# Kernel optimization log

Hardware: AMD Instinct MI355X
Metric: run time of the kernel (lower is better)

## Reference

```python
import jax, jax.numpy as jnp
import numpy as np

D_MODEL = 1024
NHEAD = 16
HEAD_DIM = D_MODEL // NHEAD
SCALE = 1.0 / np.sqrt(HEAD_DIM).astype(np.float32)
B, L = 2, 2048
NEG_INF = -1e30


def setup_inputs() -> dict:
    key = jax.random.key(0)
    ks = jax.random.split(key, 12)
    xav = np.sqrt(6.0 / (D_MODEL + D_MODEL)).astype(np.float32)  # xavier_uniform gain=1
    def lin_w(k):
        return jax.random.uniform(k, (D_MODEL, D_MODEL), jnp.float32, -xav, xav)
    x = jax.random.normal(ks[0], (B, L, D_MODEL), jnp.float32)
    role_mask = jax.random.randint(ks[1], (B, L), 0, 2, jnp.int32)
    # causal attention mask: True = masked (upper triangle above diagonal)
    attn_mask = jnp.triu(jnp.ones((L, L), jnp.bool_), k=1)
    # random key padding: True = padded key
    key_padding_mask = jax.random.randint(ks[2], (B, L), 0, 2, jnp.int32).astype(jnp.bool_)
    return {
        "x": x,
        "role_mask": role_mask,
        "attn_mask": attn_mask,
        "key_padding_mask": key_padding_mask,
        "Wq": lin_w(ks[3]), "bq": jnp.zeros((D_MODEL,), jnp.float32),
        "Wk": lin_w(ks[4]), "bk": jnp.zeros((D_MODEL,), jnp.float32),
        "Wv": lin_w(ks[5]), "bv": jnp.zeros((D_MODEL,), jnp.float32),
        "Wo": lin_w(ks[6]), "bo": jnp.zeros((D_MODEL,), jnp.float32),
        "delta": jnp.asarray(1.0, jnp.float32),
    }


def reference(x, role_mask, attn_mask, key_padding_mask,
              Wq, bq, Wk, bk, Wv, bv, Wo, bo, delta):
    Bb, Ll, Dd = x.shape
    def heads(t):  # [B,L,D] -> [B,H,L,hd]
        return t.reshape(Bb, Ll, NHEAD, HEAD_DIM).transpose(0, 2, 1, 3)
    Q = heads(x @ Wq.T + bq)
    K = heads(x @ Wk.T + bk)
    V = heads(x @ Wv.T + bv)
    scores = jnp.einsum('bhqd,bhkd->bhqk', Q, K) * SCALE  # [B,H,L,L]
    same_role = (role_mask[:, :, None] == role_mask[:, None, :])  # [B,L,L]
    scores = scores + (same_role.astype(scores.dtype) * delta)[:, None, :, :]
    scores = jnp.where(attn_mask[None, None, :, :], -jnp.inf, scores)
    scores = jnp.where(key_padding_mask[:, None, None, :], -jnp.inf, scores)
    attn = jax.nn.softmax(scores, axis=-1)
    attn = jnp.nan_to_num(attn, nan=0.0, posinf=0.0, neginf=0.0)
    out = jnp.einsum('bhqk,bhkd->bhqd', attn, V)
    out = out.transpose(0, 2, 1, 3).reshape(Bb, Ll, Dd)
    return out @ Wo.T + bo
```

## Files before the change

kernel.cpp:

```cpp
#include <hip/hip_runtime.h>
#include <hip/hip_bf16.h>

#define DM 1024
#define NH 16
#define HD 64
#define BB 2
#define LL 2048
#define SCALE 0.125f
#define NEG_BIG -1e30f
#define LOG2E 1.4426950408889634f
#define SC2 (SCALE * LOG2E)
#define FIXM 16.0f
#define SLOTB 8448
#define POOL0_SLOTS 960

typedef __bf16 bf16;
typedef __bf16 bf16x8 __attribute__((ext_vector_type(8)));
typedef __bf16 bf16x4 __attribute__((ext_vector_type(4)));
typedef float f32x4 __attribute__((ext_vector_type(4)));

static __device__ inline bf16x8 load8(const bf16* p) {
    return *reinterpret_cast<const bf16x8*>(p);
}

static __device__ inline float scrub(float x) {
    union { float f; unsigned u; } c; c.f = x;
    return ((c.u & 0x7F800000u) == 0x7F800000u) ? 0.f : x;
}

typedef __attribute__((address_space(1))) const unsigned char ga_t;
typedef __attribute__((address_space(3))) unsigned char ls_t;
static __device__ inline void gload_lds16(const void* g, void* l) {
    __builtin_amdgcn_global_load_lds((ga_t*)g, (ls_t*)l, 16, 0, 0);
}

__global__ __launch_bounds__(256) void prep_all(
    const float* __restrict__ x,
    const float* __restrict__ Wq, const float* __restrict__ Wk,
    const float* __restrict__ Wv, const float* __restrict__ Wo,
    bf16* __restrict__ xb, bf16* __restrict__ Wqb, bf16* __restrict__ Wkb,
    bf16* __restrict__ Wvb, bf16* __restrict__ Wob,
    const int* __restrict__ role, const void* __restrict__ kpad,
    const float* __restrict__ deltap, float2* __restrict__ biasG)
{
    const int tid = threadIdx.x;
    const int gid = blockIdx.x;
    if (gid < 2048) {
        const float* src; bf16* dst; size_t base;
        if (gid < 1024) { src = x; dst = xb; base = (size_t)gid * 1024; }
        else {
            const int wsel = (gid - 1024) >> 8;
            src = (wsel == 0) ? Wq : (wsel == 1) ? Wk : (wsel == 2) ? Wv : Wo;
            dst = (wsel == 0) ? Wqb : (wsel == 1) ? Wkb : (wsel == 2) ? Wvb : Wob;
            base = (size_t)((gid - 1024) & 255) * 1024;
        }
#pragma unroll
        for (int it = 0; it < 4; it++) {
            const size_t i = base + it * 256 + tid;
            const f32x4 v = ((const f32x4*)src)[i];
            bf16x4 o;
            o[0] = (bf16)v[0]; o[1] = (bf16)v[1]; o[2] = (bf16)v[2]; o[3] = (bf16)v[3];
            ((bf16x4*)dst)[i] = o;
        }
        return;
    }
    const unsigned char* kb = (const unsigned char*)kpad;
    int f3F = 0, fLow = 0, fOff = 0;
    for (int i = (tid & 63); i < BB * LL; i += 64) {
        const unsigned char v = kb[i];
        if (v == 0x3F) f3F = 1;
        if ((i & 3) < 2 && v) fLow = 1;
        if ((i & 3) && v) fOff = 1;
    }
    const int mode = __any(f3F) ? (__any(fLow) ? 3 : 2) : (__any(fOff) ? 1 : 0);
    const float d2 = scrub(deltap[0]) * LOG2E;
    const int idx = (gid - 2048) * 256 + tid;
    const bool pad = (mode == 0) ? (((const int*)kpad)[idx] != 0)
                   : (mode == 1) ? (((const unsigned char*)kpad)[idx] != 0)
                   : (mode == 2) ? (((const float*)kpad)[idx] != 0.f)
                                 : (((const unsigned short*)kpad)[idx] != 0);
    const int r = role[idx];
    const float base = (pad ? NEG_BIG : 0.f) - FIXM;
    float2 o;
    o.x = base + ((r == 0) ? d2 : 0.f);
    o.y = base + ((r == 1) ? d2 : 0.f);
    biasG[idx] = o;
}

__global__ __launch_bounds__(256) void qkv_bf16(
    const bf16* __restrict__ xb,
    const bf16* __restrict__ Wqb, const bf16* __restrict__ Wkb, const bf16* __restrict__ Wvb,
    const float* __restrict__ bq, const float* __restrict__ bk, const float* __restrict__ bv,
    bf16* __restrict__ qw, bf16* __restrict__ kw, bf16* __restrict__ vw)
{
    __shared__ bf16 As[128 * 32];
    __shared__ bf16 Bs[128 * 32];
    const int tid = threadIdx.x;
    const int lane = tid & 63, w = tid >> 6;
    const int wm = w >> 1, wn = w & 1;
    const int ln = lane & 15, quad = lane >> 4;

    const int m0 = blockIdx.x * 128;
    const int sel = blockIdx.y >> 3;
    const int nloc0 = (blockIdx.y & 7) * 128;

    const bf16* Wb = (sel == 0) ? Wqb : ((sel == 1) ? Wkb : Wvb);
    const float* bias = (sel == 0) ? bq : ((sel == 1) ? bk : bv);

    const int rA = lane >> 2;
    const int cA = (lane & 3) * 8;

    f32x4 acc[4][4] = {};
    for (int k0 = 0; k0 < DM; k0 += 32) {
        __syncthreads();
#pragma unroll
        for (int s = 0; s < 2; s++) {
            const int r0 = s * 64 + w * 16;
            gload_lds16(xb + (size_t)(m0 + r0 + rA) * DM + k0 + cA, &As[r0 * 32]);
            gload_lds16(Wb + (size_t)(nloc0 + r0 + rA) * DM + k0 + cA, &Bs[r0 * 32]);
        }
        __syncthreads();
        bf16x8 a[4], b[4];
#pragma unroll
        for (int mi = 0; mi < 4; mi++)
            a[mi] = *(bf16x8*)&As[(wm * 64 + mi * 16 + ln) * 32 + quad * 8];
#pragma unroll
        for (int ni = 0; ni < 4; ni++)
            b[ni] = *(bf16x8*)&Bs[(wn * 64 + ni * 16 + ln) * 32 + quad * 8];
#pragma unroll
        for (int mi = 0; mi < 4; mi++)
#pragma unroll
            for (int ni = 0; ni < 4; ni++)
                acc[mi][ni] = __builtin_amdgcn_mfma_f32_16x16x32_bf16(a[mi], b[ni], acc[mi][ni], 0, 0, 0);
    }

#pragma unroll
    for (int mi = 0; mi < 4; mi++) {
#pragma unroll
        for (int ni = 0; ni < 4; ni++) {
            const int ncol = nloc0 + wn * 64 + ni * 16 + ln;
            const float bv_ = bias[ncol];
            const int hh = ncol >> 6, dd = ncol & 63;
#pragma unroll
            for (int i = 0; i < 4; i++) {
                const int row = m0 + wm * 64 + mi * 16 + quad * 4 + i;
                const int bb = row >> 11, llr = row & (LL - 1);
                const bf16 v = (bf16)scrub(acc[mi][ni][i] + bv_);
                const size_t idx = (((size_t)(bb * NH + hh) * LL) + llr) * HD + dd;
                if (sel == 0)      qw[idx] = v;
                else if (sel == 1) kw[idx] = v;
                else               vw[idx] = v;
            }
        }
    }
}

__global__ __launch_bounds__(256) void vtrans(
    const bf16* __restrict__ vw, bf16* __restrict__ vtw)
{
    __shared__ bf16 T[64 * 72];
    const int tid = threadIdx.x;
    const int bh = blockIdx.x >> 5;
    const int l0 = (blockIdx.x & 31) * 64;
    const size_t base = (size_t)bh * LL * HD;

#pragma unroll
    for (int pass = 0; pass < 2; pass++) {
        const int e = pass * 2048 + tid * 8;
        const int r = e >> 6, c = e & 63;
        *(bf16x8*)&T[r * 72 + c] = load8(vw + base + (size_t)(l0 + r) * HD + c);
    }
    __syncthreads();
#pragma unroll
    for (int pass = 0; pass < 2; pass++) {
        const int e = pass * 2048 + tid * 8;
        const int d = e >> 6, lc = e & 63;
        bf16x8 v;
#pragma unroll
        for (int j = 0; j < 8; j++) v[j] = T[(lc + j) * 72 + d];
        *(bf16x8*)(vtw + base + (size_t)d * LL + l0 + lc) = v;
    }
}

#define PSTR 40
__global__ __launch_bounds__(256) void attn_v7(
    const bf16* __restrict__ qw, const bf16* __restrict__ kw, const bf16* __restrict__ vtw,
    const int* __restrict__ role, const float2* __restrict__ biasG,
    char* __restrict__ pool0, char* __restrict__ pool1,
    bf16* __restrict__ attn_out)
{
    const int qb = 31 - (blockIdx.x / 3);
    const int c = blockIdx.x % 3;
    const int nch = (qb + 12) / 12;
    if (c >= nch) return;

    __shared__ bf16 Ks[2][2][64 * 32];
    __shared__ bf16 Vs[2][2][64 * 32];
    __shared__ bf16 Ps[4][2][16 * PSTR];

    const int tid = threadIdx.x;
    const int lane = tid & 63, w = tid >> 6;
    const int col = lane & 15, quad = lane >> 4;
    const int bh = blockIdx.y;
    const int h = bh & (NH - 1), b = bh >> 4;
    const int q0 = qb * 64 + w * 16;

    const bf16* qbase = qw + (size_t)((b * NH + h) * LL) * HD;
    const bf16* kbase = kw + (size_t)((b * NH + h) * LL) * HD;
    const bf16* vbase = vtw + (size_t)((b * NH + h) * HD) * LL;
    const float2* bias2 = biasG + (size_t)b * LL;
    const int* rrow = role + b * LL;

    const int srow = lane >> 2;
    const int scol = (lane & 3) * 8;
    const bf16* ksrc = kbase + (size_t)(w * 16 + srow) * HD + scol;
    const bf16* vsrc = vbase + (size_t)(w * 16 + srow) * LL + scol;

    bf16x8 qf[2];
    qf[0] = load8(qbase + (size_t)(q0 + col) * HD + quad * 8);
    qf[1] = load8(qbase + (size_t)(q0 + col) * HD + 32 + quad * 8);

    int role_q[4];
#pragma unroll
    for (int i = 0; i < 4; i++) role_q[i] = rrow[q0 + quad * 4 + i];

    float lacc[4] = {0.f, 0.f, 0.f, 0.f};
    f32x4 o[4] = {};

    const int t0 = c * 12;
    const int t1 = (t0 + 12 < qb + 1) ? t0 + 12 : qb + 1;

    {
        const int kp = t0 * 64;
#pragma unroll
        for (int st = 0; st < 2; st++)
            gload_lds16(ksrc + (size_t)kp * HD + st * 32, &Ks[0][st][w * 512]);
#pragma unroll
        for (int kh = 0; kh < 2; kh++)
            gload_lds16(vsrc + kp + kh * 32, &Vs[0][kh][w * 512]);
    }

    for (int kt = t0; kt < t1; kt++) {
        const int cur = (kt - t0) & 1;
        __syncthreads();

        if (kt + 1 < t1) {
            const int k1 = (kt + 1) * 64;
#pragma unroll
            for (int st = 0; st < 2; st++)
                gload_lds16(ksrc + (size_t)k1 * HD + st * 32, &Ks[cur ^ 1][st][w * 512]);
#pragma unroll
            for (int kh = 0; kh < 2; kh++)
                gload_lds16(vsrc + k1 + kh * 32, &Vs[cur ^ 1][kh][w * 512]);
        }

        const int k0 = kt * 64;
        float2 bb[4];
#pragma unroll
        for (int ns = 0; ns < 4; ns++) bb[ns] = bias2[k0 + ns * 16 + col];

        f32x4 s[4] = {};
#pragma unroll
        for (int st = 0; st < 2; st++) {
#pragma unroll
            for (int ns = 0; ns < 4; ns++) {
                const bf16x8 kf = *(bf16x8*)&Ks[cur][st][(ns * 16 + col) * 32 + quad * 8];
                s[ns] = __builtin_amdgcn_mfma_f32_16x16x32_bf16(qf[st], kf, s[ns], 0, 0, 0);
            }
        }
        const bool diag = (kt == qb);
#pragma unroll
        for (int ns = 0; ns < 4; ns++) {
            const int kk = k0 + ns * 16 + col;
#pragma unroll
            for (int i = 0; i < 4; i++) {
                float sv = fmaf(s[ns][i], SC2, role_q[i] ? bb[ns].y : bb[ns].x);
                if (diag && kk > q0 + quad * 4 + i) sv = NEG_BIG;
                const float p = exp2f(fminf(sv, 14.f));
                lacc[i] += p;
                Ps[w][ns >> 1][(quad * 4 + i) * PSTR + (ns & 1) * 16 + col] = (bf16)p;
            }
        }
        bf16x8 pf[2];
#pragma unroll
        for (int st = 0; st < 2; st++)
            pf[st] = *(bf16x8*)&Ps[w][st][col * PSTR + quad * 8];
#pragma unroll
        for (int ns = 0; ns < 4; ns++) {
#pragma unroll
            for (int kh = 0; kh < 2; kh++) {
                const bf16x8 vf = *(bf16x8*)&Vs[cur][kh][(ns * 16 + col) * 32 + quad * 8];
                o[ns] = __builtin_amdgcn_mfma_f32_16x16x32_bf16(pf[kh], vf, o[ns], 0, 0, 0);
            }
        }
    }

    if (nch == 1) {
        bf16* orow = attn_out + (size_t)(b * LL) * DM;
#pragma unroll
        for (int i = 0; i < 4; i++) {
            float l = lacc[i];
#pragma unroll
            for (int off = 8; off > 0; off >>= 1)
                l += __shfl_xor(l, off, 16);
            const float inv = (l > 0.f) ? 1.f / l : 0.f;
            const int qq = q0 + quad * 4 + i;
#pragma unroll
            for (int ns = 0; ns < 4; ns++)
                orow[(size_t)qq * DM + h * HD + ns * 16 + col] = (bf16)scrub(o[ns][i] * inv);
        }
    } else {
        const int base = (qb <= 23) ? (qb - 12) * 2 : 24 + (qb - 24) * 3;
        const int slot = bh * 48 + base + c;
        char* ptr = (slot < POOL0_SLOTS) ? (pool0 + (size_t)slot * SLOTB)
                                         : (pool1 + (size_t)(slot - POOL0_SLOTS) * SLOTB);
        bf16* op = (bf16*)ptr;
        float* lp = (float*)(ptr + 8192);
#pragma unroll
        for (int i = 0; i < 4; i++) {
            float l = lacc[i];
#pragma unroll
            for (int off = 8; off > 0; off >>= 1)
                l += __shfl_xor(l, off, 16);
            const int r = w * 16 + quad * 4 + i;
            if (col == 0) lp[r] = l;
#pragma unroll
            for (int ns = 0; ns < 4; ns++)
                op[r * 64 + ns * 16 + col] = (bf16)scrub(o[ns][i]);
        }
    }
}

__global__ __launch_bounds__(256) void combine(
    const char* __restrict__ pool0, const char* __restrict__ pool1,
    bf16* __restrict__ attn_out)
{
    const int qb = 12 + blockIdx.x;
    const int bh = blockIdx.y;
    const int h = bh & (NH - 1), b = bh >> 4;
    const int nch = (qb + 12) / 12;
    const int base = (qb <= 23) ? (qb - 12) * 2 : 24 + (qb - 24) * 3;

    const char* ptr[3];
    for (int c = 0; c < nch; c++) {
        const int slot = bh * 48 + base + c;
        ptr[c] = (slot < POOL0_SLOTS) ? (pool0 + (size_t)slot * SLOTB)
                                      : (pool1 + (size_t)(slot - POOL0_SLOTS) * SLOTB);
    }

    __shared__ float linv[64];
    const int tid = threadIdx.x;
    if (tid < 64) {
        float ls = 0.f;
        for (int c = 0; c < nch; c++) ls += ((const float*)(ptr[c] + 8192))[tid];
        linv[tid] = (ls > 0.f) ? 1.f / ls : 0.f;
    }
    __syncthreads();

    const int r = tid >> 2;
    const int d0 = (tid & 3) * 16;
    float acc[16] = {};
    for (int c = 0; c < nch; c++) {
        const bf16* op = (const bf16*)ptr[c];
#pragma unroll
        for (int half = 0; half < 2; half++) {
            const bf16x8 v = load8(op + r * 64 + d0 + half * 8);
#pragma unroll
            for (int j = 0; j < 8; j++) acc[half * 8 + j] += (float)v[j];
        }
    }
    const float inv = linv[r];
    bf16x8 outv[2];
#pragma unroll
    for (int half = 0; half < 2; half++)
#pragma unroll
        for (int j = 0; j < 8; j++)
            outv[half][j] = (bf16)scrub(acc[half * 8 + j] * inv);
    bf16* orow = attn_out + ((size_t)(b * LL) + qb * 64 + r) * DM + h * HD + d0;
    *(bf16x8*)orow = outv[0];
    *(bf16x8*)(orow + 8) = outv[1];
}

__global__ __launch_bounds__(256) void out_bf16(
    const bf16* __restrict__ A, const bf16* __restrict__ Wb,
    const float* __restrict__ bias, float* __restrict__ out)
{
    __shared__ bf16 As[128 * 32];
    __shared__ bf16 Bs[64 * 32];
    const int tid = threadIdx.x;
    const int lane = tid & 63, w = tid >> 6;
    const int ln = lane & 15, quad = lane >> 4;
    const int m0 = blockIdx.x * 128;
    const int n0 = blockIdx.y * 64;

    const int rA = lane >> 2;
    const int cA = (lane & 3) * 8;

    f32x4 acc[2][4] = {};
    for (int k0 = 0; k0 < DM; k0 += 32) {
        __syncthreads();
#pragma unroll
        for (int s = 0; s < 2; s++) {
            const int r0 = s * 64 + w * 16;
            gload_lds16(A + (size_t)(m0 + r0 + rA) * DM + k0 + cA, &As[r0 * 32]);
        }
        gload_lds16(Wb + (size_t)(n0 + w * 16 + rA) * DM + k0 + cA, &Bs[w * 16 * 32]);
        __syncthreads();
        bf16x8 a[2], b[4];
#pragma unroll
        for (int mi = 0; mi < 2; mi++)
            a[mi] = *(bf16x8*)&As[(w * 32 + mi * 16 + ln) * 32 + quad * 8];
#pragma unroll
        for (int ni = 0; ni < 4; ni++)
            b[ni] = *(bf16x8*)&Bs[(ni * 16 + ln) * 32 + quad * 8];
#pragma unroll
        for (int mi = 0; mi < 2; mi++)
#pragma unroll
            for (int ni = 0; ni < 4; ni++)
                acc[mi][ni] = __builtin_amdgcn_mfma_f32_16x16x32_bf16(a[mi], b[ni], acc[mi][ni], 0, 0, 0);
    }
#pragma unroll
    for (int mi = 0; mi < 2; mi++) {
#pragma unroll
        for (int ni = 0; ni < 4; ni++) {
            const int ncol = n0 + ni * 16 + ln;
            const float bv_ = bias[ncol];
#pragma unroll
            for (int i = 0; i < 4; i++) {
                const int row = m0 + w * 32 + mi * 16 + quad * 4 + i;
                out[(size_t)row * DM + ncol] = scrub(acc[mi][ni][i] + bv_);
            }
        }
    }
}

extern "C" void kernel_launch(void* const* d_in, const int* in_sizes, int n_in,
                              void* d_out, int out_size, void* d_ws, size_t ws_size,
                              hipStream_t stream) {
    const float* x    = (const float*)d_in[0];
    const int*   role = (const int*)d_in[1];
    const void*  kpad = d_in[3];
    const float* Wq = (const float*)d_in[4];
    const float* bq = (const float*)d_in[5];
    const float* Wk = (const float*)d_in[6];
    const float* bk = (const float*)d_in[7];
    const float* Wv = (const float*)d_in[8];
    const float* bv = (const float*)d_in[9];
    const float* Wo = (const float*)d_in[10];
    const float* bo = (const float*)d_in[11];
    const float* dl = (const float*)d_in[12];

    char* ws = (char*)d_ws;
    bf16* qw   = (bf16*)(ws);
    bf16* kw   = (bf16*)(ws + (size_t)(8u  << 20));
    bf16* vnat = (bf16*)(ws + (size_t)(16u << 20));
    bf16* aw   = (bf16*)(ws + (size_t)(24u << 20));
    bf16* xb   = (bf16*)(ws + (size_t)(32u << 20));
    bf16* vtw  = xb;
    bf16* Wqb  = (bf16*)(ws + (size_t)(40u << 20));
    bf16* Wkb  = (bf16*)(ws + (size_t)(42u << 20));
    bf16* Wvb  = (bf16*)(ws + (size_t)(44u << 20));
    bf16* Wob  = (bf16*)(ws + (size_t)(46u << 20));
    float2* biasG = (float2*)(ws + (size_t)(48u << 20));
    char* pool0 = (char*)vnat;
    char* pool1 = (char*)Wqb;
    float* out = (float*)d_out;

    prep_all<<<dim3(2064), dim3(256), 0, stream>>>(
        x, Wq, Wk, Wv, Wo, xb, Wqb, Wkb, Wvb, Wob, role, kpad, dl, biasG);
    qkv_bf16<<<dim3(32, 24), dim3(256), 0, stream>>>(xb, Wqb, Wkb, Wvb, bq, bk, bv, qw, kw, vnat);
    vtrans<<<dim3(BB * NH * (LL / 64)), dim3(256), 0, stream>>>(vnat, vtw);
    attn_v7<<<dim3(96, 32), dim3(256), 0, stream>>>(qw, kw, vtw, role, biasG, pool0, pool1, aw);
    combine<<<dim3(20, 32), dim3(256), 0, stream>>>(pool0, pool1, aw);
    out_bf16<<<dim3(32, 16), dim3(256), 0, stream>>>(aw, Wob, bo, out);
}
```

Before: 260.5 us.

## Fuse fp32-to-bf16 conversion into GEMMs and write V transposed directly

Removes the separate conversion pass by having the QKV and output GEMMs load fp32 x/weights and convert to bf16 while staging into LDS. The QKV epilogue writes V directly in transposed layout, which eliminates the vtrans kernel. The mask/bias prep blocks are folded into the QKV launch, and the attention grid is compacted to 60 columns so no blocks exit immediately. This saves launches and intermediate traffic, but the GEMMs now read twice the bytes through register loads instead of async LDS loads, and the transposed V stores are strided.

```diff
diff --git a/kernel.cpp b/kernel.cpp
--- a/kernel.cpp
+++ b/kernel.cpp
@@ -23,6 +23,15 @@
     return *reinterpret_cast<const bf16x8*>(p);
 }
 
+static __device__ inline bf16x8 cvt8(const float* p) {
+    const f32x4 a = *reinterpret_cast<const f32x4*>(p);
+    const f32x4 b = *reinterpret_cast<const f32x4*>(p + 4);
+    bf16x8 r;
+    r[0] = (bf16)a[0]; r[1] = (bf16)a[1]; r[2] = (bf16)a[2]; r[3] = (bf16)a[3];
+    r[4] = (bf16)b[0]; r[5] = (bf16)b[1]; r[6] = (bf16)b[2]; r[7] = (bf16)b[3];
+    return r;
+}
+
 static __device__ inline float scrub(float x) {
     union { float f; unsigned u; } c; c.f = x;
     return ((c.u & 0x7F800000u) == 0x7F800000u) ? 0.f : x;
@@ -34,90 +43,68 @@
     __builtin_amdgcn_global_load_lds((ga_t*)g, (ls_t*)l, 16, 0, 0);
 }
 
-__global__ __launch_bounds__(256) void prep_all(
+__global__ __launch_bounds__(256) void qkv_mega(
     const float* __restrict__ x,
-    const float* __restrict__ Wq, const float* __restrict__ Wk,
-    const float* __restrict__ Wv, const float* __restrict__ Wo,
-    bf16* __restrict__ xb, bf16* __restrict__ Wqb, bf16* __restrict__ Wkb,
-    bf16* __restrict__ Wvb, bf16* __restrict__ Wob,
+    const float* __restrict__ Wq, const float* __restrict__ Wk, const float* __restrict__ Wv,
+    const float* __restrict__ bq, const float* __restrict__ bk, const float* __restrict__ bv,
     const int* __restrict__ role, const void* __restrict__ kpad,
-    const float* __restrict__ deltap, float2* __restrict__ biasG)
+    const float* __restrict__ deltap,
+    bf16* __restrict__ qw, bf16* __restrict__ kw, bf16* __restrict__ vtw,
+    float2* __restrict__ biasG)
 {
     const int tid = threadIdx.x;
-    const int gid = blockIdx.x;
-    if (gid < 2048) {
-        const float* src; bf16* dst; size_t base;
-        if (gid < 1024) { src = x; dst = xb; base = (size_t)gid * 1024; }
-        else {
-            const int wsel = (gid - 1024) >> 8;
-            src = (wsel == 0) ? Wq : (wsel == 1) ? Wk : (wsel == 2) ? Wv : Wo;
-            dst = (wsel == 0) ? Wqb : (wsel == 1) ? Wkb : (wsel == 2) ? Wvb : Wob;
-            base = (size_t)((gid - 1024) & 255) * 1024;
-        }
-#pragma unroll
-        for (int it = 0; it < 4; it++) {
-            const size_t i = base + it * 256 + tid;
-            const f32x4 v = ((const f32x4*)src)[i];
-            bf16x4 o;
-            o[0] = (bf16)v[0]; o[1] = (bf16)v[1]; o[2] = (bf16)v[2]; o[3] = (bf16)v[3];
-            ((bf16x4*)dst)[i] = o;
-        }
+    const int g = blockIdx.x;
+
+    if (g >= 768) {
+        const unsigned char* kb = (const unsigned char*)kpad;
+        int f3F = 0, fLow = 0, fOff = 0;
+        for (int i = (tid & 63); i < BB * LL; i += 64) {
+            const unsigned char v = kb[i];
+            if (v == 0x3F) f3F = 1;
+            if ((i & 3) < 2 && v) fLow = 1;
+            if ((i & 3) && v) fOff = 1;
+        }
+        const int mode = __any(f3F) ? (__any(fLow) ? 3 : 2) : (__any(fOff) ? 1 : 0);
+        const float d2 = scrub(deltap[0]) * LOG2E;
+        const int idx = (g - 768) * 256 + tid;
+        const bool pad = (mode == 0) ? (((const int*)kpad)[idx] != 0)
+                       : (mode == 1) ? (((const unsigned char*)kpad)[idx] != 0)
+                       : (mode == 2) ? (((const float*)kpad)[idx] != 0.f)
+                                     : (((const unsigned short*)kpad)[idx] != 0);
+        const int r = role[idx];
+        const float base = (pad ? NEG_BIG : 0.f) - FIXM;
+        float2 o;
+        o.x = base + ((r == 0) ? d2 : 0.f);
+        o.y = base + ((r == 1) ? d2 : 0.f);
+        biasG[idx] = o;
         return;
     }
-    const unsigned char* kb = (const unsigned char*)kpad;
-    int f3F = 0, fLow = 0, fOff = 0;
-    for (int i = (tid & 63); i < BB * LL; i += 64) {
-        const unsigned char v = kb[i];
-        if (v == 0x3F) f3F = 1;
-        if ((i & 3) < 2 && v) fLow = 1;
-        if ((i & 3) && v) fOff = 1;
-    }
-    const int mode = __any(f3F) ? (__any(fLow) ? 3 : 2) : (__any(fOff) ? 1 : 0);
-    const float d2 = scrub(deltap[0]) * LOG2E;
-    const int idx = (gid - 2048) * 256 + tid;
-    const bool pad = (mode == 0) ? (((const int*)kpad)[idx] != 0)
-                   : (mode == 1) ? (((const unsigned char*)kpad)[idx] != 0)
-                   : (mode == 2) ? (((const float*)kpad)[idx] != 0.f)
-                                 : (((const unsigned short*)kpad)[idx] != 0);
-    const int r = role[idx];
-    const float base = (pad ? NEG_BIG : 0.f) - FIXM;
-    float2 o;
-    o.x = base + ((r == 0) ? d2 : 0.f);
-    o.y = base + ((r == 1) ? d2 : 0.f);
-    biasG[idx] = o;
-}
-
-__global__ __launch_bounds__(256) void qkv_bf16(
-    const bf16* __restrict__ xb,
-    const bf16* __restrict__ Wqb, const bf16* __restrict__ Wkb, const bf16* __restrict__ Wvb,
-    const float* __restrict__ bq, const float* __restrict__ bk, const float* __restrict__ bv,
-    bf16* __restrict__ qw, bf16* __restrict__ kw, bf16* __restrict__ vw)
-{
+
     __shared__ bf16 As[128 * 32];
     __shared__ bf16 Bs[128 * 32];
-    const int tid = threadIdx.x;
     const int lane = tid & 63, w = tid >> 6;
     const int wm = w >> 1, wn = w & 1;
     const int ln = lane & 15, quad = lane >> 4;
 
-    const int m0 = blockIdx.x * 128;
-    const int sel = blockIdx.y >> 3;
-    const int nloc0 = (blockIdx.y & 7) * 128;
-
-    const bf16* Wb = (sel == 0) ? Wqb : ((sel == 1) ? Wkb : Wvb);
+    const int m0 = (g & 31) * 128;
+    const int by = g >> 5;
+    const int sel = by >> 3;
+    const int nloc0 = (by & 7) * 128;
+
+    const float* W    = (sel == 0) ? Wq : ((sel == 1) ? Wk : Wv);
     const float* bias = (sel == 0) ? bq : ((sel == 1) ? bk : bv);
 
-    const int rA = lane >> 2;
-    const int cA = (lane & 3) * 8;
+    const int srow = tid >> 2;
+    const int scb  = (tid & 3) * 8;
 
     f32x4 acc[4][4] = {};
     for (int k0 = 0; k0 < DM; k0 += 32) {
         __syncthreads();
 #pragma unroll
-        for (int s = 0; s < 2; s++) {
-            const int r0 = s * 64 + w * 16;
-            gload_lds16(xb + (size_t)(m0 + r0 + rA) * DM + k0 + cA, &As[r0 * 32]);
-            gload_lds16(Wb + (size_t)(nloc0 + r0 + rA) * DM + k0 + cA, &Bs[r0 * 32]);
+        for (int p = 0; p < 2; p++) {
+            const int row = p * 64 + srow;
+            *(bf16x8*)&As[row * 32 + scb] = cvt8(x + (size_t)(m0 + row) * DM + k0 + scb);
+            *(bf16x8*)&Bs[row * 32 + scb] = cvt8(W + (size_t)(nloc0 + row) * DM + k0 + scb);
         }
         __syncthreads();
         bf16x8 a[4], b[4];
@@ -146,53 +133,30 @@
                 const int row = m0 + wm * 64 + mi * 16 + quad * 4 + i;
                 const int bb = row >> 11, llr = row & (LL - 1);
                 const bf16 v = (bf16)scrub(acc[mi][ni][i] + bv_);
-                const size_t idx = (((size_t)(bb * NH + hh) * LL) + llr) * HD + dd;
-                if (sel == 0)      qw[idx] = v;
-                else if (sel == 1) kw[idx] = v;
-                else               vw[idx] = v;
+                if (sel == 0)
+                    qw[(((size_t)(bb * NH + hh) * LL) + llr) * HD + dd] = v;
+                else if (sel == 1)
+                    kw[(((size_t)(bb * NH + hh) * LL) + llr) * HD + dd] = v;
+                else
+                    vtw[(((size_t)(bb * NH + hh) * HD) + dd) * LL + llr] = v;
             }
         }
     }
 }
 
-__global__ __launch_bounds__(256) void vtrans(
-    const bf16* __restrict__ vw, bf16* __restrict__ vtw)
-{
-    __shared__ bf16 T[64 * 72];
-    const int tid = threadIdx.x;
-    const int bh = blockIdx.x >> 5;
-    const int l0 = (blockIdx.x & 31) * 64;
-    const size_t base = (size_t)bh * LL * HD;
-
-#pragma unroll
-    for (int pass = 0; pass < 2; pass++) {
-        const int e = pass * 2048 + tid * 8;
-        const int r = e >> 6, c = e & 63;
-        *(bf16x8*)&T[r * 72 + c] = load8(vw + base + (size_t)(l0 + r) * HD + c);
-    }
-    __syncthreads();
-#pragma unroll
-    for (int pass = 0; pass < 2; pass++) {
-        const int e = pass * 2048 + tid * 8;
-        const int d = e >> 6, lc = e & 63;
-        bf16x8 v;
-#pragma unroll
-        for (int j = 0; j < 8; j++) v[j] = T[(lc + j) * 72 + d];
-        *(bf16x8*)(vtw + base + (size_t)d * LL + l0 + lc) = v;
-    }
-}
-
 #define PSTR 40
-__global__ __launch_bounds__(256) void attn_v7(
+__global__ __launch_bounds__(256) void attn_v8(
     const bf16* __restrict__ qw, const bf16* __restrict__ kw, const bf16* __restrict__ vtw,
     const int* __restrict__ role, const float2* __restrict__ biasG,
     char* __restrict__ pool0, char* __restrict__ pool1,
     bf16* __restrict__ attn_out)
 {
-    const int qb = 31 - (blockIdx.x / 3);
-    const int c = blockIdx.x % 3;
+    const int xg = blockIdx.x;
+    int qb, c;
+    if (xg < 24)      { qb = 31 - xg / 3; c = xg % 3; }
+    else if (xg < 48) { qb = 23 - (xg - 24) / 2; c = (xg - 24) % 2; }
+    else              { qb = 59 - xg; c = 0; }
     const int nch = (qb + 12) / 12;
-    if (c >= nch) return;
 
     __shared__ bf16 Ks[2][2][64 * 32];
     __shared__ bf16 Vs[2][2][64 * 32];
@@ -381,8 +345,8 @@
     *(bf16x8*)(orow + 8) = outv[1];
 }
 
-__global__ __launch_bounds__(256) void out_bf16(
-    const bf16* __restrict__ A, const bf16* __restrict__ Wb,
+__global__ __launch_bounds__(256) void out_mega(
+    const bf16* __restrict__ A, const float* __restrict__ Wo,
     const float* __restrict__ bias, float* __restrict__ out)
 {
     __shared__ bf16 As[128 * 32];
@@ -395,6 +359,8 @@
 
     const int rA = lane >> 2;
     const int cA = (lane & 3) * 8;
+    const int srow = tid >> 2;
+    const int scb  = (tid & 3) * 8;
 
     f32x4 acc[2][4] = {};
     for (int k0 = 0; k0 < DM; k0 += 32) {
@@ -404,7 +370,7 @@
             const int r0 = s * 64 + w * 16;
             gload_lds16(A + (size_t)(m0 + r0 + rA) * DM + k0 + cA, &As[r0 * 32]);
         }
-        gload_lds16(Wb + (size_t)(n0 + w * 16 + rA) * DM + k0 + cA, &Bs[w * 16 * 32]);
+        *(bf16x8*)&Bs[srow * 32 + scb] = cvt8(Wo + (size_t)(n0 + srow) * DM + k0 + scb);
         __syncthreads();
         bf16x8 a[2], b[4];
 #pragma unroll
@@ -453,24 +419,17 @@
     char* ws = (char*)d_ws;
     bf16* qw   = (bf16*)(ws);
     bf16* kw   = (bf16*)(ws + (size_t)(8u  << 20));
-    bf16* vnat = (bf16*)(ws + (size_t)(16u << 20));
+    char* pool0 = ws + (size_t)(16u << 20);
     bf16* aw   = (bf16*)(ws + (size_t)(24u << 20));
-    bf16* xb   = (bf16*)(ws + (size_t)(32u << 20));
-    bf16* vtw  = xb;
-    bf16* Wqb  = (bf16*)(ws + (size_t)(40u << 20));
-    bf16* Wkb  = (bf16*)(ws + (size_t)(42u << 20));
-    bf16* Wvb  = (bf16*)(ws + (size_t)(44u << 20));
-    bf16* Wob  = (bf16*)(ws + (size_t)(46u << 20));
+    bf16* vtw  = (bf16*)(ws + (size_t)(32u << 20));
+    char* pool1 = ws + (size_t)(40u << 20);
     float2* biasG = (float2*)(ws + (size_t)(48u << 20));
-    char* pool0 = (char*)vnat;
-    char* pool1 = (char*)Wqb;
     float* out = (float*)d_out;
 
-    prep_all<<<dim3(2064), dim3(256), 0, stream>>>(
-        x, Wq, Wk, Wv, Wo, xb, Wqb, Wkb, Wvb, Wob, role, kpad, dl, biasG);
-    qkv_bf16<<<dim3(32, 24), dim3(256), 0, stream>>>(xb, Wqb, Wkb, Wvb, bq, bk, bv, qw, kw, vnat);
-    vtrans<<<dim3(BB * NH * (LL / 64)), dim3(256), 0, stream>>>(vnat, vtw);
-    attn_v7<<<dim3(96, 32), dim3(256), 0, stream>>>(qw, kw, vtw, role, biasG, pool0, pool1, aw);
+    qkv_mega<<<dim3(784), dim3(256), 0, stream>>>(
+        x, Wq, Wk, Wv, bq, bk, bv, role, kpad, dl, qw, kw, vtw, biasG);
+    attn_v8<<<dim3(60, 32), dim3(256), 0, stream>>>(
+        qw, kw, vtw, role, biasG, pool0, pool1, aw);
     combine<<<dim3(20, 32), dim3(256), 0, stream>>>(pool0, pool1, aw);
-    out_bf16<<<dim3(32, 16), dim3(256), 0, stream>>>(aw, Wob, bo, out);
-}
+    out_mega<<<dim3(32, 16), dim3(256), 0, stream>>>(aw, Wo, bo, out);
+}
```

New measurement: 257.7 us. About the same (-1.1%).

## Fuse V transpose into QKV epilogue, vectorize P stores, compact attention grid

Applied to the files above, without the earlier changes.

The QKV projection now writes V straight into a transposed layout with a permuted key order inside each 64-key tile, so the separate vtrans kernel and its extra global round trip are dropped. In the attention kernel, P values are packed four at a time into bf16x4 stores using the matching permuted layout and a smaller LDS stride, in place of scalar LDS writes. The grid shrinks from 96 to 60 blocks per head by mapping block indices only to the (query block, chunk) pairs that do work, so no blocks launch just to exit. The workspace layout is rearranged to fit, and the transposed V stores from the GEMM epilogue are scattered, which may cost write efficiency.

```diff
diff --git a/kernel.cpp b/kernel.cpp
--- a/kernel.cpp
+++ b/kernel.cpp
@@ -91,7 +91,7 @@
     const bf16* __restrict__ xb,
     const bf16* __restrict__ Wqb, const bf16* __restrict__ Wkb, const bf16* __restrict__ Wvb,
     const float* __restrict__ bq, const float* __restrict__ bk, const float* __restrict__ bv,
-    bf16* __restrict__ qw, bf16* __restrict__ kw, bf16* __restrict__ vw)
+    bf16* __restrict__ qw, bf16* __restrict__ kw, bf16* __restrict__ vtw)
 {
     __shared__ bf16 As[128 * 32];
     __shared__ bf16 Bs[128 * 32];
@@ -146,53 +146,33 @@
                 const int row = m0 + wm * 64 + mi * 16 + quad * 4 + i;
                 const int bb = row >> 11, llr = row & (LL - 1);
                 const bf16 v = (bf16)scrub(acc[mi][ni][i] + bv_);
-                const size_t idx = (((size_t)(bb * NH + hh) * LL) + llr) * HD + dd;
-                if (sel == 0)      qw[idx] = v;
-                else if (sel == 1) kw[idx] = v;
-                else               vw[idx] = v;
+                if (sel == 0)
+                    qw[(((size_t)(bb * NH + hh) * LL) + llr) * HD + dd] = v;
+                else if (sel == 1)
+                    kw[(((size_t)(bb * NH + hh) * LL) + llr) * HD + dd] = v;
+                else {
+                    const int kl = llr & 63;
+                    const int pos = (llr & ~63) + ((kl & 15) * 4 + (kl >> 4));
+                    vtw[(((size_t)(bb * NH + hh) * HD) + dd) * LL + pos] = v;
+                }
             }
         }
     }
 }
 
-__global__ __launch_bounds__(256) void vtrans(
-    const bf16* __restrict__ vw, bf16* __restrict__ vtw)
-{
-    __shared__ bf16 T[64 * 72];
-    const int tid = threadIdx.x;
-    const int bh = blockIdx.x >> 5;
-    const int l0 = (blockIdx.x & 31) * 64;
-    const size_t base = (size_t)bh * LL * HD;
-
-#pragma unroll
-    for (int pass = 0; pass < 2; pass++) {
-        const int e = pass * 2048 + tid * 8;
-        const int r = e >> 6, c = e & 63;
-        *(bf16x8*)&T[r * 72 + c] = load8(vw + base + (size_t)(l0 + r) * HD + c);
-    }
-    __syncthreads();
-#pragma unroll
-    for (int pass = 0; pass < 2; pass++) {
-        const int e = pass * 2048 + tid * 8;
-        const int d = e >> 6, lc = e & 63;
-        bf16x8 v;
-#pragma unroll
-        for (int j = 0; j < 8; j++) v[j] = T[(lc + j) * 72 + d];
-        *(bf16x8*)(vtw + base + (size_t)d * LL + l0 + lc) = v;
-    }
-}
-
-#define PSTR 40
-__global__ __launch_bounds__(256) void attn_v7(
+#define PSTR 36
+__global__ __launch_bounds__(256) void attn_v9(
     const bf16* __restrict__ qw, const bf16* __restrict__ kw, const bf16* __restrict__ vtw,
     const int* __restrict__ role, const float2* __restrict__ biasG,
     char* __restrict__ pool0, char* __restrict__ pool1,
     bf16* __restrict__ attn_out)
 {
-    const int qb = 31 - (blockIdx.x / 3);
-    const int c = blockIdx.x % 3;
+    const int xg = blockIdx.x;
+    int qb, c;
+    if (xg < 24)      { qb = 31 - xg / 3; c = xg % 3; }
+    else if (xg < 48) { qb = 23 - (xg - 24) / 2; c = (xg - 24) % 2; }
+    else              { qb = 59 - xg; c = 0; }
     const int nch = (qb + 12) / 12;
-    if (c >= nch) return;
 
     __shared__ bf16 Ks[2][2][64 * 32];
     __shared__ bf16 Vs[2][2][64 * 32];
@@ -269,17 +249,20 @@
             }
         }
         const bool diag = (kt == qb);
-#pragma unroll
-        for (int ns = 0; ns < 4; ns++) {
-            const int kk = k0 + ns * 16 + col;
-#pragma unroll
-            for (int i = 0; i < 4; i++) {
+        const int half = col >> 3;
+        const int poff = (col & 7) * 4;
+#pragma unroll
+        for (int i = 0; i < 4; i++) {
+            bf16x4 pk;
+#pragma unroll
+            for (int ns = 0; ns < 4; ns++) {
                 float sv = fmaf(s[ns][i], SC2, role_q[i] ? bb[ns].y : bb[ns].x);
-                if (diag && kk > q0 + quad * 4 + i) sv = NEG_BIG;
+                if (diag && (k0 + ns * 16 + col) > q0 + quad * 4 + i) sv = NEG_BIG;
                 const float p = exp2f(fminf(sv, 14.f));
                 lacc[i] += p;
-                Ps[w][ns >> 1][(quad * 4 + i) * PSTR + (ns & 1) * 16 + col] = (bf16)p;
+                pk[ns] = (bf16)p;
             }
+            *(bf16x4*)&Ps[w][half][(quad * 4 + i) * PSTR + poff] = pk;
         }
         bf16x8 pf[2];
 #pragma unroll
@@ -453,24 +436,24 @@
     char* ws = (char*)d_ws;
     bf16* qw   = (bf16*)(ws);
     bf16* kw   = (bf16*)(ws + (size_t)(8u  << 20));
-    bf16* vnat = (bf16*)(ws + (size_t)(16u << 20));
+    bf16* Wqb  = (bf16*)(ws + (size_t)(16u << 20));
+    bf16* Wkb  = (bf16*)(ws + (size_t)(18u << 20));
+    bf16* Wvb  = (bf16*)(ws + (size_t)(20u << 20));
+    char* pool0 = ws + (size_t)(16u << 20);
     bf16* aw   = (bf16*)(ws + (size_t)(24u << 20));
-    bf16* xb   = (bf16*)(ws + (size_t)(32u << 20));
-    bf16* vtw  = xb;
-    bf16* Wqb  = (bf16*)(ws + (size_t)(40u << 20));
-    bf16* Wkb  = (bf16*)(ws + (size_t)(42u << 20));
-    bf16* Wvb  = (bf16*)(ws + (size_t)(44u << 20));
-    bf16* Wob  = (bf16*)(ws + (size_t)(46u << 20));
+    bf16* vtw  = (bf16*)(ws + (size_t)(32u << 20));
+    bf16* xb   = (bf16*)(ws + (size_t)(40u << 20));
+    char* pool1 = ws + (size_t)(40u << 20);
+    bf16* Wob  = (bf16*)(ws + (size_t)(48u << 20) + 65536);
     float2* biasG = (float2*)(ws + (size_t)(48u << 20));
-    char* pool0 = (char*)vnat;
-    char* pool1 = (char*)Wqb;
     float* out = (float*)d_out;
 
     prep_all<<<dim3(2064), dim3(256), 0, stream>>>(
         x, Wq, Wk, Wv, Wo, xb, Wqb, Wkb, Wvb, Wob, role, kpad, dl, biasG);
-    qkv_bf16<<<dim3(32, 24), dim3(256), 0, stream>>>(xb, Wqb, Wkb, Wvb, bq, bk, bv, qw, kw, vnat);
-    vtrans<<<dim3(BB * NH * (LL / 64)), dim3(256), 0, stream>>>(vnat, vtw);
-    attn_v7<<<dim3(96, 32), dim3(256), 0, stream>>>(qw, kw, vtw, role, biasG, pool0, pool1, aw);
+    qkv_bf16<<<dim3(32, 24), dim3(256), 0, stream>>>(
+        xb, Wqb, Wkb, Wvb, bq, bk, bv, qw, kw, vtw);
+    attn_v9<<<dim3(60, 32), dim3(256), 0, stream>>>(
+        qw, kw, vtw, role, biasG, pool0, pool1, aw);
     combine<<<dim3(20, 32), dim3(256), 0, stream>>>(pool0, pool1, aw);
     out_bf16<<<dim3(32, 16), dim3(256), 0, stream>>>(aw, Wob, bo, out);
 }
```

Result: faster. 246.3 us, median of 2 (-5.4%).
